# Kernel tuning notes

Measured on AMD Instinct MI355X. Metric: run time of the kernel, lower is better.

Reference implementation:

```python
import jax, jax.numpy as jnp
import numpy as np
from jax import lax

LP, LQ, B, IN = 512, 256, 32, 512
H = 150  # hidden_size*2 hardcoded in module


def setup_inputs() -> dict:
    key = jax.random.key(0)
    ks = jax.random.split(key, 12)
    s = 0.05  # keep tanh/sigmoid unsaturated
    return {
        "up": jax.random.normal(ks[0], (LP, B, IN), jnp.float32),
        "uq": jax.random.normal(ks[1], (LQ, B, IN), jnp.float32),
        "v0": jax.random.normal(ks[2], (B, H), jnp.float32),
        "V": jax.random.normal(ks[3], (B, H), jnp.float32),
        "Wp": jax.random.normal(ks[4], (H, 2 * IN), jnp.float32) * s,
        "Wq": jax.random.normal(ks[5], (H, 2 * IN), jnp.float32) * s,
        "Wv": jax.random.normal(ks[6], (H, H), jnp.float32) * s,
        "Wg": jax.random.normal(ks[7], (4 * IN, 4 * IN), jnp.float32) * s,
        "W_ih": jax.random.normal(ks[8], (3 * H, 2 * IN), jnp.float32) * s,
        "W_hh": jax.random.normal(ks[9], (3 * H, H), jnp.float32) * s,
        "b_ih": jax.random.normal(ks[10], (3 * H,), jnp.float32) * s,
        "b_hh": jax.random.normal(ks[11], (3 * H,), jnp.float32) * s,
    }


def reference(up, uq, v0, V, Wp, Wq, Wv, Wg, W_ih, W_hh, b_ih, b_hh):
    in2 = up.shape[2] * 2
    Up = jnp.concatenate([up, up], axis=2)          # [lp, B, 2*in]
    Uq = jnp.concatenate([uq, uq], axis=2)          # [lq, B, 2*in]
    WqUq = jnp.einsum("qbi,hi->qbh", Uq, Wq)        # hoisted: constant over steps

    def step(v, Up_i):
        Wup = Up_i @ Wp.T                            # [B, H]
        x = jnp.tanh(Wup + WqUq + v @ Wv.T)          # [lq, B, H]
        s = jnp.einsum("qbh,bh->bq", x, V)           # attention logits [B, lq]
        a = jax.nn.softmax(s, axis=1)
        c = jnp.einsum("bq,qbi->bi", a, Uq)          # context [B, 2*in]
        r = jnp.concatenate([Up_i, c], axis=1)       # [B, 4*in]
        g = jax.nn.sigmoid(r @ Wg.T)
        r = g * r
        c_ = r[:, in2:]                              # gated context [B, 2*in]
        # GRUCell
        gi = c_ @ W_ih.T + b_ih
        gh = v @ W_hh.T + b_hh
        i_r, i_z, i_n = jnp.split(gi, 3, axis=1)
        h_r, h_z, h_n = jnp.split(gh, 3, axis=1)
        rg = jax.nn.sigmoid(i_r + h_r)
        zg = jax.nn.sigmoid(i_z + h_z)
        ng = jnp.tanh(i_n + rg * h_n)
        v_new = (1.0 - zg) * ng + zg * v
        return v_new, v_new

    _, vs = lax.scan(step, v0, Up)                   # vs: [lp, B, H]
    return vs  # dropout = identity (eval)
```

## Files before the change

kernel.cpp:

```cpp
#include <hip/hip_runtime.h>
#include <hip/hip_bf16.h>

#define AGENT __HIP_MEMORY_SCOPE_AGENT
#define RLX __ATOMIC_RELAXED
typedef unsigned long long u64t;

typedef _Float16 h2 __attribute__((ext_vector_type(2)));
union U32H2 { unsigned u; h2 h; };
__device__ __forceinline__ h2 uh(unsigned u){ U32H2 c; c.u=u; return c.h; }
__device__ __forceinline__ unsigned pk(float a, float b){
  U32H2 c; c.h = h2{(_Float16)a, (_Float16)b}; return c.u;
}
#define RCPF(x) __builtin_amdgcn_rcpf(x)

__device__ __forceinline__ float DOT2(unsigned a, unsigned b, float acc){
#if __has_builtin(__builtin_amdgcn_fdot2)
  return __builtin_amdgcn_fdot2(uh(a), uh(b), acc, false);
#else
  h2 x = uh(a), y = uh(b);
  acc = fmaf((float)x[0], (float)y[0], acc);
  return fmaf((float)x[1], (float)y[1], acc);
#endif
}
__device__ __forceinline__ float sigm(float x){ return RCPF(1.0f+__expf(-x)); }
__device__ __forceinline__ float ftanh(float x){ return 1.0f - 2.0f*RCPF(1.0f+__expf(x+x)); }

__device__ __forceinline__ void pubw(u64t* p, unsigned seq, unsigned data){
  __hip_atomic_store(p, ((u64t)seq<<32)|(u64t)data, RLX, AGENT);
}
template<int K>
__device__ __forceinline__ void waitN(const u64t* base, const int* off, unsigned seq,
                                      unsigned* out, unsigned* kf){
  long n=0;
  for(;;){
    u64t v[K]; bool ok=true;
    #pragma unroll
    for(int k=0;k<K;k++) v[k]=__hip_atomic_load(base+off[k], RLX, AGENT);
    #pragma unroll
    for(int k=0;k<K;k++) ok &= ((unsigned)(v[k]>>32)==seq);
    if(ok){
      #pragma unroll
      for(int k=0;k<K;k++) out[k]=(unsigned)v[k];
      return;
    }
    __builtin_amdgcn_s_sleep(1);
    if((++n&63)==0){
      if(__hip_atomic_load(kf,RLX,AGENT)!=0u) break;
      if(n>300000L){ __hip_atomic_store(kf,1u,RLX,AGENT); break; }
    }
  }
  #pragma unroll
  for(int k=0;k<K;k++) out[k]=0u;
}

__global__ void k_fold(const float* __restrict__ Wp, const float* __restrict__ Wq,
                       const float* __restrict__ Wg,
                       float* __restrict__ WpT, float* __restrict__ WqT,
                       float* __restrict__ WgupT, float* __restrict__ WgcT)
{
  int i0 = blockIdx.x*blockDim.x+threadIdx.x;
  int st = gridDim.x*blockDim.x;
  for(int o=i0;o<512*150;o+=st){ int h=o%150, i=o/150;
    WpT[o]=Wp[h*1024+i]+Wp[h*1024+512+i];
    WqT[o]=Wq[h*1024+i]+Wq[h*1024+512+i]; }
  for(int o=i0;o<512*1024;o+=st){ int i=o&511, j=o>>9;
    size_t rb=(size_t)(1024+j)*2048;
    WgupT[(size_t)i*1024+j]=Wg[rb+i]+Wg[rb+512+i];
    WgcT [(size_t)i*1024+j]=Wg[rb+1024+i]+Wg[rb+1536+i]; }
}

__global__ void k_fold2(const float* __restrict__ Wih,
                        const float* __restrict__ Whh, const float* __restrict__ Wv,
                        unsigned* __restrict__ WihT,
                        unsigned* __restrict__ WhhP, unsigned* __restrict__ WvU)
{
  int i0 = blockIdx.x*blockDim.x+threadIdx.x;
  int st = gridDim.x*blockDim.x;
  for(int o=i0;o<512*450;o+=st){ int k=o%450, jp=o/450;
    WihT[(size_t)jp*456+k] = pk(Wih[(size_t)k*1024+2*jp], Wih[(size_t)k*1024+2*jp+1]); }
  for(int o=i0;o<76*456;o+=st){ int k=o%456, p=o/456;
    float x=0.f,y=0.f;
    if(k<450){ if(2*p<150) x=Whh[k*150+2*p]; if(2*p+1<150) y=Whh[k*150+2*p+1]; }
    WhhP[o]=pk(x,y); }
  for(int o=i0;o<76*152;o+=st){ int h=o%152, p=o/152;
    float x=0.f,y=0.f;
    if(h<150){ if(2*p<150) x=Wv[h*150+2*p]; if(2*p+1<150) y=Wv[h*150+2*p+1]; }
    WvU[o]=pk(x,y); }
}

__global__ __launch_bounds__(256) void k_uqp(const float* __restrict__ uq, unsigned* __restrict__ uqP){
  __shared__ float Al[32*512];
  int b = blockIdx.x, qt = blockIdx.y, tid = threadIdx.x;
  for(int o4=tid;o4<4096;o4+=256){ int m=o4>>7, i4=o4&127;
    ((float4*)Al)[o4] = *(const float4*)&uq[(size_t)(qt*32+m)*16384 + b*512 + i4*4]; }
  __syncthreads();
  for(int o=tid;o<8192;o+=256){ int i=o>>4, p=o&15;
    uqP[((size_t)b*512+i)*128 + qt*16 + p] = pk(Al[(2*p)*512+i], Al[(2*p+1)*512+i]); }
}

template<int MODE>
__global__ __launch_bounds__(256) void k_gemm(const float* __restrict__ A,
   const float* __restrict__ WT, _Float16* __restrict__ oH, int N)
{
  __shared__ float Al[32*512];
  int mt=blockIdx.x, nt=blockIdx.y, tid=threadIdx.x;
  const float* Ab = A + (size_t)mt*16384;
  for(int o=tid;o<4096;o+=256) ((float4*)Al)[o]=((const float4*)Ab)[o];
  __syncthreads();
  int n = nt*256+tid;
  if(n>=N) return;
  float acc[32];
  #pragma unroll
  for(int m=0;m<32;m++) acc[m]=0.f;
  const float* wp = WT + n;
  #pragma unroll 2
  for(int k=0;k<512;k+=2){
    float w0 = wp[(size_t)k*N], w1 = wp[(size_t)(k+1)*N];
    #pragma unroll
    for(int m=0;m<32;m++) acc[m]=fmaf(w0, Al[m*512+k], acc[m]);
    #pragma unroll
    for(int m=0;m<32;m++) acc[m]=fmaf(w1, Al[m*512+k+1], acc[m]);
  }
  if(MODE==0){
    #pragma unroll
    for(int m=0;m<32;m++) oH[((size_t)m*512 + mt)*152 + n] = (_Float16)acc[m];
  } else if(MODE==3){
    #pragma unroll
    for(int m=0;m<32;m++) oH[((size_t)m*256 + mt)*152 + n] = (_Float16)acc[m];
  } else {
    #pragma unroll
    for(int m=0;m<32;m++) oH[((size_t)m*512 + mt)*1024 + n] = (_Float16)acc[m];
  }
}

__global__ __launch_bounds__(256) void k_gemmM(const float* __restrict__ uq,
   const float* __restrict__ WgcT, unsigned* __restrict__ Mp)
{
  __shared__ float Al[32*512];
  int b=blockIdx.x, qt=blockIdx.y, nt=blockIdx.z, tid=threadIdx.x;
  for(int o4=tid;o4<4096;o4+=256){ int m=o4>>7, i4=o4&127;
    ((float4*)Al)[o4] = *(const float4*)&uq[(size_t)(qt*32+m)*16384 + b*512 + i4*4]; }
  __syncthreads();
  int n = nt*256+tid;
  float acc[32];
  #pragma unroll
  for(int m=0;m<32;m++) acc[m]=0.f;
  const float* wp = WgcT + n;
  #pragma unroll 2
  for(int k=0;k<512;k+=2){
    float w0 = wp[(size_t)k*1024], w1 = wp[(size_t)(k+1)*1024];
    #pragma unroll
    for(int m=0;m<32;m++) acc[m]=fmaf(w0, Al[m*512+k], acc[m]);
    #pragma unroll
    for(int m=0;m<32;m++) acc[m]=fmaf(w1, Al[m*512+k+1], acc[m]);
  }
  #pragma unroll
  for(int p=0;p<16;p++)
    Mp[((size_t)b*1024 + n)*128 + qt*16 + p] = pk(acc[2*p], acc[2*p+1]);
}

__global__ void k_init(unsigned* comm){
  int i = blockIdx.x*blockDim.x + threadIdx.x;
  if(i < 123920) comm[i] = 0u;
}

struct __align__(16) SMO {
  unsigned WvU[76*152];
  unsigned WqUq[256*76];
  unsigned wup[80], vp[80];
  float V[152], v[152], w2[152], s[256], a[256];
  float gi[452], rgh[2][452], bi[452], bh[452];
};
struct __align__(16) SMW {
  unsigned M[128*257];
  unsigned a2[128], gup[128], cpr[128];
  float ccf[128], Gc[256], c_f[256], rgi[2][452];
};
union SMU { SMO o; SMW w; };

__global__ __launch_bounds__(1024) void persist(
  const unsigned* __restrict__ uqP,   const unsigned* __restrict__ Mp,
  const unsigned* __restrict__ Gup3u, const unsigned* __restrict__ Wuphu,
  const unsigned* __restrict__ WqUqhu, const unsigned* __restrict__ WihTu,
  const unsigned* __restrict__ WhhP,  const unsigned* __restrict__ WvUg,
  const float* __restrict__ v0, const float* __restrict__ Vin,
  const float* __restrict__ bih, const float* __restrict__ bhh,
  u64t* aP, u64t* giP, unsigned* kf,
  float* __restrict__ dout)
{
  extern __shared__ char smraw[];
  SMU& S = *reinterpret_cast<SMU*>(smraw);
  const int tid = threadIdx.x;
  const int bid = blockIdx.x;

  if(bid < 32){
    const int b = bid;
    for(int o=tid;o<11552;o+=1024) S.o.WvU[o]=WvUg[o];
    for(int o=tid;o<19456;o+=1024){ int q=o/76,w=o%76;
      S.o.WqUq[o]=WqUqhu[((size_t)b*256+q)*76+w]; }
    for(int o=tid;o<152;o+=1024){
      S.o.V[o]=(o<150)?Vin[b*150+o]:0.f;
      S.o.v[o]=(o<150)?v0[b*150+o]:0.f; }
    for(int o=tid;o<452;o+=1024){
      S.o.bi[o]=(o<450)?bih[o]:0.f;
      S.o.bh[o]=(o<450)?bhh[o]:0.f; }
    __syncthreads();

    const int gibase = b*1808;
    for(int t=0;t<512;++t){
      if(tid<76) S.o.wup[tid]=Wuphu[((size_t)b*512+t)*76+tid];
      if(t>0){
        if(tid<450){
          int off[4]={gibase+tid, gibase+452+tid, gibase+904+tid, gibase+1356+tid};
          unsigned gv[4];
          waitN<4>(giP,off,(unsigned)t,gv,kf);
          S.o.gi[tid]=__uint_as_float(gv[0])+__uint_as_float(gv[1])
                     +__uint_as_float(gv[2])+__uint_as_float(gv[3]);
        }
        __syncthreads();
        if(tid<150){
          float gh0=S.o.rgh[0][tid]+S.o.rgh[1][tid]+S.o.bh[tid];
          float gh1=S.o.rgh[0][150+tid]+S.o.rgh[1][150+tid]+S.o.bh[150+tid];
          float gh2=S.o.rgh[0][300+tid]+S.o.rgh[1][300+tid]+S.o.bh[300+tid];
          float rg=sigm(S.o.gi[tid]+S.o.bi[tid] + gh0);
          float zg=sigm(S.o.gi[150+tid]+S.o.bi[150+tid] + gh1);
          float ng=ftanh(S.o.gi[300+tid]+S.o.bi[300+tid] + rg*gh2);
          float vn=fmaf(zg, S.o.v[tid]-ng, ng);
          S.o.v[tid]=vn;
          dout[((size_t)(t-1)*32+b)*150+tid]=vn;
        }
        __syncthreads();
      }
      if(tid<76) S.o.vp[tid]=pk(S.o.v[2*tid], S.o.v[2*tid+1]);
      __syncthreads();
      if(tid<608){
        int h=tid>>2, qd=tid&3;
        float acc=0.f;
        if(h<150){
          #pragma unroll
          for(int p=qd*19;p<qd*19+19;p++) acc=DOT2(S.o.WvU[p*152+h], S.o.vp[p], acc);
        }
        acc+=__shfl_xor(acc,1,64); acc+=__shfl_xor(acc,2,64);
        if(h<150&&qd==0){ h2 ww=uh(S.o.wup[h>>1]); S.o.w2[h]=acc+(float)ww[h&1]; }
      }
      __syncthreads();
      {
        int q=tid>>2, hq=tid&3;
        int hp0=hq*19, hp1=(hq==3)?75:hp0+19;
        float acc=0.f;
        for(int hp=hp0;hp<hp1;hp++){
          h2 wp=uh(S.o.WqUq[q*76+hp]);
          acc=fmaf(S.o.V[2*hp],   ftanh(S.o.w2[2*hp]  +(float)wp[0]), acc);
          acc=fmaf(S.o.V[2*hp+1], ftanh(S.o.w2[2*hp+1]+(float)wp[1]), acc);
        }
        acc+=__shfl_xor(acc,1,64); acc+=__shfl_xor(acc,2,64);
        if(hq==0) S.o.s[q]=acc;
      }
      __syncthreads();
      if(tid<64){
        float x0=S.o.s[tid],x1=S.o.s[tid+64],x2=S.o.s[tid+128],x3=S.o.s[tid+192];
        float mx=fmaxf(fmaxf(x0,x1),fmaxf(x2,x3));
        #pragma unroll
        for(int o=1;o<64;o<<=1) mx=fmaxf(mx,__shfl_xor(mx,o,64));
        float e0=__expf(x0-mx),e1=__expf(x1-mx),e2=__expf(x2-mx),e3=__expf(x3-mx);
        float sm=e0+e1+e2+e3;
        #pragma unroll
        for(int o=1;o<64;o<<=1) sm+=__shfl_xor(sm,o,64);
        float rs=RCPF(sm);
        S.o.a[tid]=e0*rs; S.o.a[tid+64]=e1*rs; S.o.a[tid+128]=e2*rs; S.o.a[tid+192]=e3*rs;
      }
      __syncthreads();
      if(tid<128) pubw(aP+b*128+tid,(unsigned)(t+1), pk(S.o.a[2*tid],S.o.a[2*tid+1]));
      {
        int k=tid&511, half=tid>>9;
        float ah=0.f;
        if(k<450){
          int p0=half*38, p1=half?76:38;
          for(int p=p0;p<p1;p++) ah=DOT2(WhhP[p*456+k], S.o.vp[p], ah);
          S.o.rgh[half][k]=ah;
        }
      }
    }
    if(tid<450){
      int off[4]={gibase+tid, gibase+452+tid, gibase+904+tid, gibase+1356+tid};
      unsigned gv[4];
      waitN<4>(giP,off,512u,gv,kf);
      S.o.gi[tid]=__uint_as_float(gv[0])+__uint_as_float(gv[1])
                 +__uint_as_float(gv[2])+__uint_as_float(gv[3]);
    }
    __syncthreads();
    if(tid<150){
      float gh0=S.o.rgh[0][tid]+S.o.rgh[1][tid]+S.o.bh[tid];
      float gh1=S.o.rgh[0][150+tid]+S.o.rgh[1][150+tid]+S.o.bh[150+tid];
      float gh2=S.o.rgh[0][300+tid]+S.o.rgh[1][300+tid]+S.o.bh[300+tid];
      float rg=sigm(S.o.gi[tid]+S.o.bi[tid] + gh0);
      float zg=sigm(S.o.gi[150+tid]+S.o.bi[150+tid] + gh1);
      float ng=ftanh(S.o.gi[300+tid]+S.o.bi[300+tid] + rg*gh2);
      dout[((size_t)511*32+b)*150+tid]=fmaf(zg, S.o.v[tid]-ng, ng);
    }

  } else {
    const int wid = bid-32;
    const int b = wid>>2, s = wid&3;
    for(int o=tid;o<32768;o+=1024){
      int qp=o&127, jl=o>>7;
      int j = s*128 + (jl&127) + ((jl>>7)<<9);
      S.w.M[qp*257+jl] = Mp[((size_t)b*1024+j)*128+qp];
    }
    __syncthreads();
    const size_t uqbase = ((size_t)b*512 + s*128)*128;
    for(int t=0;t<512;++t){
      if(tid<128){
        int wi = (tid<64)? (s*64+tid) : (256+s*64+tid-64);
        S.w.gup[tid] = Gup3u[((size_t)b*512+t)*512 + wi];
      }
      if(tid<128){
        int off[1]={b*128+tid};
        unsigned av[1];
        waitN<1>(aP,off,(unsigned)(t+1),av,kf);
        S.w.a2[tid]=av[0];
      }
      __syncthreads();
      {
        int i=tid>>3, q8=tid&7;
        float acc=0.f;
        const unsigned* up = uqP + uqbase + (size_t)i*128;
        #pragma unroll 4
        for(int kk=0;kk<16;kk++){
          int qp=kk*8+q8;
          acc=DOT2(S.w.a2[qp], up[qp], acc);
        }
        acc+=__shfl_xor(acc,1,64); acc+=__shfl_xor(acc,2,64); acc+=__shfl_xor(acc,4,64);
        if(q8==0) S.w.ccf[i]=acc;
      }
      {
        int jl=tid>>2, qc=tid&3;
        float acc=0.f;
        #pragma unroll 8
        for(int kk=0;kk<32;kk++){
          int qp=kk*4+qc;
          acc=DOT2(S.w.a2[qp], S.w.M[qp*257+jl], acc);
        }
        acc+=__shfl_xor(acc,1,64); acc+=__shfl_xor(acc,2,64);
        if(qc==0) S.w.Gc[jl]=acc;
      }
      __syncthreads();
      if(tid<256){
        h2 gv=uh(S.w.gup[tid>>1]);
        float g=sigm(S.w.Gc[tid]+(float)gv[tid&1]);
        S.w.c_f[tid]=g*S.w.ccf[tid&127];
      }
      __syncthreads();
      if(tid<128) S.w.cpr[tid]=pk(S.w.c_f[2*tid],S.w.c_f[2*tid+1]);
      __syncthreads();
      {
        int k=tid&511, half=tid>>9;
        float acc=0.f;
        if(k<450){
          #pragma unroll 4
          for(int m=0;m<64;m++){
            int jpg = half*256 + s*64 + m;
            acc=DOT2(WihTu[(size_t)jpg*456+k], S.w.cpr[half*64+m], acc);
          }
          S.w.rgi[half][k]=acc;
        }
      }
      __syncthreads();
      if(tid<450)
        pubw(giP + ((size_t)b*4+s)*452 + tid, (unsigned)(t+1),
             __float_as_uint(S.w.rgi[0][tid]+S.w.rgi[1][tid]));
    }
  }
}

extern "C" void kernel_launch(void* const* d_in, const int* in_sizes, int n_in,
                              void* d_out, int out_size, void* d_ws, size_t ws_size,
                              hipStream_t stream)
{
  const float* up  = (const float*)d_in[0];
  const float* uq  = (const float*)d_in[1];
  const float* v0  = (const float*)d_in[2];
  const float* Vm  = (const float*)d_in[3];
  const float* Wp  = (const float*)d_in[4];
  const float* Wq  = (const float*)d_in[5];
  const float* Wv  = (const float*)d_in[6];
  const float* Wg  = (const float*)d_in[7];
  const float* W_ih= (const float*)d_in[8];
  const float* W_hh= (const float*)d_in[9];
  const float* b_ih= (const float*)d_in[10];
  const float* b_hh= (const float*)d_in[11];
  float* dout = (float*)d_out;
  char* wsb = (char*)d_ws;

  size_t off = 0;
  auto alloc = [&](size_t bytes)->size_t{ size_t p = off; off = (off + bytes + 255) & ~(size_t)255; return p; };
  size_t oWgupT = alloc((size_t)512*1024*4);
  size_t oWgcT  = alloc((size_t)512*1024*4);
  size_t oWuph  = alloc((size_t)32*512*152*2);
  size_t oWqUqh = alloc((size_t)32*256*152*2);
  size_t oWihT  = alloc((size_t)512*456*4);
  size_t oWhhP  = alloc((size_t)76*456*4);
  size_t oWvU   = alloc((size_t)76*152*4);
  size_t oUqP   = alloc((size_t)32*512*128*4);
  size_t oMp    = alloc((size_t)32*1024*128*4);
  size_t oGup3  = alloc((size_t)32*512*1024*2);
  if(ws_size < off) return;

  float*    WgupT = (float*)(wsb + oWgupT);
  float*    WgcT  = (float*)(wsb + oWgcT);
  _Float16* Wuph  = (_Float16*)(wsb + oWuph);
  _Float16* WqUqh = (_Float16*)(wsb + oWqUqh);
  unsigned* WihT  = (unsigned*)(wsb + oWihT);
  unsigned* WhhP  = (unsigned*)(wsb + oWhhP);
  unsigned* WvU   = (unsigned*)(wsb + oWvU);
  unsigned* uqP   = (unsigned*)(wsb + oUqP);
  unsigned* Mp    = (unsigned*)(wsb + oMp);
  _Float16* Gup3  = (_Float16*)(wsb + oGup3);
  float* WpT = (float*)(wsb + oGup3);
  float* WqT = (float*)(wsb + oGup3 + 307456);

  u64t* comm64 = (u64t*)(wsb + oWgupT);
  u64t* aP  = comm64;
  u64t* giP = comm64 + 4096;
  unsigned* kf = (unsigned*)(comm64 + 61952);

  k_fold <<<256,256,0,stream>>>(Wp,Wq,Wg, WpT,WqT,WgupT,WgcT);
  k_fold2<<<256,256,0,stream>>>(W_ih, W_hh, Wv, WihT, WhhP, WvU);
  k_uqp  <<<dim3(32,8),256,0,stream>>>(uq, uqP);
  k_gemm<0><<<dim3(512,1),256,0,stream>>>(up, WpT, Wuph, 150);
  k_gemm<3><<<dim3(256,1),256,0,stream>>>(uq, WqT, WqUqh, 150);
  k_gemm<4><<<dim3(512,4),256,0,stream>>>(up, WgupT, Gup3, 1024);
  k_gemmM<<<dim3(32,8,4),256,0,stream>>>(uq, WgcT, Mp);
  k_init <<<122,1024,0,stream>>>((unsigned*)comm64);

  int smem = (int)sizeof(SMU);
  hipFuncSetAttribute((const void*)persist, hipFuncAttributeMaxDynamicSharedMemorySize, smem);
  const unsigned* Gup3u  = (const unsigned*)Gup3;
  const unsigned* Wuphu  = (const unsigned*)Wuph;
  const unsigned* WqUqhu = (const unsigned*)WqUqh;
  void* ka[16] = { (void*)&uqP, (void*)&Mp, (void*)&Gup3u, (void*)&Wuphu, (void*)&WqUqhu,
                   (void*)&WihT, (void*)&WhhP, (void*)&WvU,
                   (void*)&v0, (void*)&Vm, (void*)&b_ih, (void*)&b_hh,
                   (void*)&aP, (void*)&giP, (void*)&kf, (void*)&dout };
  hipLaunchCooperativeKernel((const void*)persist, dim3(160), dim3(1024), ka,
                             (unsigned)smem, stream);
}
```

Before: 7.354 ms.

## Cache GRU weights in registers and pack cross-block gi partials as fp16 pairs

Loads the W_hh slice (38 packed words) and the W_ih slice (64 packed words) into per-thread registers once, instead of re-reading them from global memory every timestep. The gi partial sums exchanged between worker blocks and owner blocks are now packed as fp16 pairs, which halves the number of flag-tagged 64-bit slots polled and published per step and shrinks the comm buffer and its init. The kill-flag check in the spin-wait loop also runs less often. The risks are higher register pressure at 1024 threads per block and reduced precision in the gi accumulation from the fp16 packing.

```diff
diff --git a/kernel.cpp b/kernel.cpp
--- a/kernel.cpp
+++ b/kernel.cpp
@@ -44,7 +44,7 @@
       return;
     }
     __builtin_amdgcn_s_sleep(1);
-    if((++n&63)==0){
+    if((++n&255)==0){
       if(__hip_atomic_load(kf,RLX,AGENT)!=0u) break;
       if(n>300000L){ __hip_atomic_store(kf,1u,RLX,AGENT); break; }
     }
@@ -76,8 +76,10 @@
 {
   int i0 = blockIdx.x*blockDim.x+threadIdx.x;
   int st = gridDim.x*blockDim.x;
-  for(int o=i0;o<512*450;o+=st){ int k=o%450, jp=o/450;
-    WihT[(size_t)jp*456+k] = pk(Wih[(size_t)k*1024+2*jp], Wih[(size_t)k*1024+2*jp+1]); }
+  for(int o=i0;o<512*456;o+=st){ int k=o%456, jp=o/456;
+    unsigned v = 0u;
+    if(k<450) v = pk(Wih[(size_t)k*1024+2*jp], Wih[(size_t)k*1024+2*jp+1]);
+    WihT[o] = v; }
   for(int o=i0;o<76*456;o+=st){ int k=o%456, p=o/456;
     float x=0.f,y=0.f;
     if(k<450){ if(2*p<150) x=Whh[k*150+2*p]; if(2*p+1<150) y=Whh[k*150+2*p+1]; }
@@ -161,7 +163,7 @@
 
 __global__ void k_init(unsigned* comm){
   int i = blockIdx.x*blockDim.x + threadIdx.x;
-  if(i < 123920) comm[i] = 0u;
+  if(i < 66052) comm[i] = 0u;
 }
 
 struct __align__(16) SMO {
@@ -204,18 +206,29 @@
     for(int o=tid;o<452;o+=1024){
       S.o.bi[o]=(o<450)?bih[o]:0.f;
       S.o.bh[o]=(o<450)?bhh[o]:0.f; }
+    unsigned whh[38];
+    {
+      int k=tid&511, half=tid>>9;
+      #pragma unroll
+      for(int p=0;p<38;p++){
+        int pp=half*38+p;
+        whh[p] = (k<450 && pp<76)? WhhP[(size_t)pp*456+k] : 0u;
+      }
+    }
     __syncthreads();
 
-    const int gibase = b*1808;
+    const int gib = b*904;
     for(int t=0;t<512;++t){
       if(tid<76) S.o.wup[tid]=Wuphu[((size_t)b*512+t)*76+tid];
       if(t>0){
-        if(tid<450){
-          int off[4]={gibase+tid, gibase+452+tid, gibase+904+tid, gibase+1356+tid};
+        if(tid<225){
+          int off[4]={gib+tid, gib+226+tid, gib+452+tid, gib+678+tid};
           unsigned gv[4];
           waitN<4>(giP,off,(unsigned)t,gv,kf);
-          S.o.gi[tid]=__uint_as_float(gv[0])+__uint_as_float(gv[1])
-                     +__uint_as_float(gv[2])+__uint_as_float(gv[3]);
+          float g0=0.f,g1=0.f;
+          #pragma unroll
+          for(int k=0;k<4;k++){ h2 x=uh(gv[k]); g0+=(float)x[0]; g1+=(float)x[1]; }
+          S.o.gi[2*tid]=g0; S.o.gi[2*tid+1]=g1;
         }
         __syncthreads();
         if(tid<150){
@@ -273,20 +286,22 @@
       if(tid<128) pubw(aP+b*128+tid,(unsigned)(t+1), pk(S.o.a[2*tid],S.o.a[2*tid+1]));
       {
         int k=tid&511, half=tid>>9;
-        float ah=0.f;
         if(k<450){
-          int p0=half*38, p1=half?76:38;
-          for(int p=p0;p<p1;p++) ah=DOT2(WhhP[p*456+k], S.o.vp[p], ah);
+          float ah=0.f;
+          #pragma unroll
+          for(int p=0;p<38;p++) ah=DOT2(whh[p], S.o.vp[(half*38+p)<76 ? half*38+p : 0], ah);
           S.o.rgh[half][k]=ah;
         }
       }
     }
-    if(tid<450){
-      int off[4]={gibase+tid, gibase+452+tid, gibase+904+tid, gibase+1356+tid};
+    if(tid<225){
+      int off[4]={gib+tid, gib+226+tid, gib+452+tid, gib+678+tid};
       unsigned gv[4];
       waitN<4>(giP,off,512u,gv,kf);
-      S.o.gi[tid]=__uint_as_float(gv[0])+__uint_as_float(gv[1])
-                 +__uint_as_float(gv[2])+__uint_as_float(gv[3]);
+      float g0=0.f,g1=0.f;
+      #pragma unroll
+      for(int k=0;k<4;k++){ h2 x=uh(gv[k]); g0+=(float)x[0]; g1+=(float)x[1]; }
+      S.o.gi[2*tid]=g0; S.o.gi[2*tid+1]=g1;
     }
     __syncthreads();
     if(tid<150){
@@ -307,6 +322,15 @@
       int j = s*128 + (jl&127) + ((jl>>7)<<9);
       S.w.M[qp*257+jl] = Mp[((size_t)b*1024+j)*128+qp];
     }
+    unsigned wih[64];
+    {
+      int k=tid&511, half=tid>>9;
+      #pragma unroll
+      for(int m=0;m<64;m++){
+        int jpg = half*256 + s*64 + m;
+        wih[m] = (k<450)? WihTu[(size_t)jpg*456+k] : 0u;
+      }
+    }
     __syncthreads();
     const size_t uqbase = ((size_t)b*512 + s*128)*128;
     for(int t=0;t<512;++t){
@@ -356,19 +380,16 @@
       {
         int k=tid&511, half=tid>>9;
         float acc=0.f;
-        if(k<450){
-          #pragma unroll 4
-          for(int m=0;m<64;m++){
-            int jpg = half*256 + s*64 + m;
-            acc=DOT2(WihTu[(size_t)jpg*456+k], S.w.cpr[half*64+m], acc);
-          }
-          S.w.rgi[half][k]=acc;
-        }
-      }
-      __syncthreads();
-      if(tid<450)
-        pubw(giP + ((size_t)b*4+s)*452 + tid, (unsigned)(t+1),
-             __float_as_uint(S.w.rgi[0][tid]+S.w.rgi[1][tid]));
+        #pragma unroll
+        for(int m=0;m<64;m++) acc=DOT2(wih[m], S.w.cpr[half*64+m], acc);
+        if(k<450) S.w.rgi[half][k]=acc;
+      }
+      __syncthreads();
+      if(tid<225){
+        float g0=S.w.rgi[0][2*tid]+S.w.rgi[1][2*tid];
+        float g1=S.w.rgi[0][2*tid+1]+S.w.rgi[1][2*tid+1];
+        pubw(giP + ((size_t)b*4+s)*226 + tid, (unsigned)(t+1), pk(g0,g1));
+      }
     }
   }
 }
@@ -422,7 +443,7 @@
   u64t* comm64 = (u64t*)(wsb + oWgupT);
   u64t* aP  = comm64;
   u64t* giP = comm64 + 4096;
-  unsigned* kf = (unsigned*)(comm64 + 61952);
+  unsigned* kf = (unsigned*)(comm64 + 33024);
 
   k_fold <<<256,256,0,stream>>>(Wp,Wq,Wg, WpT,WqT,WgupT,WgcT);
   k_fold2<<<256,256,0,stream>>>(W_ih, W_hh, Wv, WihT, WhhP, WvU);
@@ -431,7 +452,7 @@
   k_gemm<3><<<dim3(256,1),256,0,stream>>>(uq, WqT, WqUqh, 150);
   k_gemm<4><<<dim3(512,4),256,0,stream>>>(up, WgupT, Gup3, 1024);
   k_gemmM<<<dim3(32,8,4),256,0,stream>>>(uq, WgcT, Mp);
-  k_init <<<122,1024,0,stream>>>((unsigned*)comm64);
+  k_init <<<65,1024,0,stream>>>((unsigned*)comm64);
 
   int smem = (int)sizeof(SMU);
   hipFuncSetAttribute((const void*)persist, hipFuncAttributeMaxDynamicSharedMemorySize, smem);
```

New measurement: 7.468 ms. Within noise of the previous version (+1.5%).
